# Kernel optimization log

Hardware: AMD Instinct MI355X
Metric: run time of the kernel (lower is better)

The kernel has to match this reference:

```python
import jax, jax.numpy as jnp
import numpy as np

B, N, D, E = 4, 8192, 8, 128
SCALE = float(1.0 / np.sqrt(E))  # torch MHA scaling, n_heads=1 -> head_dim=E


def _attn_dir(X, idx, mask, Wq, Wk, Wv, ipw, ipb, ow, ob):
    # X: [B,N,E]; idx, mask: [B,N,D]. Sequence per node = [self] + padded neighbors.
    neigh = jax.vmap(lambda x, i: x[i])(X, idx)               # [B,N,D,E] gather
    seq = jnp.concatenate([X[:, :, None, :], neigh], axis=2)  # [B,N,1+D,E]
    m = jnp.concatenate([jnp.ones(mask.shape[:2] + (1,), bool), mask.astype(bool)], axis=2)
    wq, wk, wv = jnp.split(ipw, 3, axis=0)                    # torch in_proj_weight [3E,E]
    bq, bk, bv = jnp.split(ipb, 3)
    # custom pre-projections (X @ W), then torch MHA in_proj (x @ w.T + b)
    q = (X @ Wq) @ wq.T + bq                                  # [B,N,E]; only self row queried
    k = (seq @ Wk) @ wk.T + bk                                # [B,N,1+D,E]
    v = (seq @ Wv) @ wv.T + bv                                # [B,N,1+D,E]
    scores = jnp.einsum('bne,bnse->bns', q, k) * SCALE
    scores = jnp.where(m, scores, jnp.finfo(scores.dtype).min)
    w = jax.nn.softmax(scores, axis=-1)
    ctx = jnp.einsum('bns,bnse->bne', w, v)
    return ctx @ ow.T + ob                                    # MHA out_proj


def setup_inputs():
    key = jax.random.key(0)
    ks = jax.random.split(key, 26)
    f32 = jnp.float32
    inp = {
        "X": jax.random.normal(ks[0], (B, N, E), f32),
        "in_idx": jax.random.randint(ks[1], (B, N, D), 0, N, dtype=jnp.int32),
        "out_idx": jax.random.randint(ks[2], (B, N, D), 0, N, dtype=jnp.int32),
        "in_mask": jax.random.randint(ks[3], (B, N, D), 0, 2, dtype=jnp.int32),
        "out_mask": jax.random.randint(ks[4], (B, N, D), 0, 2, dtype=jnp.int32),
    }
    i = 5
    for pfx in ("in_", "out_"):
        inp[pfx + "Wq"] = jax.random.uniform(ks[i], (E, E), f32) * 0.1; i += 1
        inp[pfx + "Wk"] = jax.random.uniform(ks[i], (E, E), f32) * 0.1; i += 1
        inp[pfx + "Wv"] = jax.random.uniform(ks[i], (E, E), f32) * 0.1; i += 1
        inp[pfx + "ipw"] = jax.random.normal(ks[i], (3 * E, E), f32) * 0.05; i += 1
        inp[pfx + "ipb"] = jax.random.normal(ks[i], (3 * E,), f32) * 0.02; i += 1
        inp[pfx + "ow"] = jax.random.normal(ks[i], (E, E), f32) * 0.05; i += 1
        inp[pfx + "ob"] = jax.random.normal(ks[i], (E,), f32) * 0.02; i += 1
    inp["lin_w"] = jax.random.normal(ks[i], (E, 2 * E), f32) * 0.05; i += 1
    inp["lin_b"] = jax.random.normal(ks[i], (E,), f32) * 0.02
    return inp


def reference(X, in_idx, out_idx, in_mask, out_mask,
              in_Wq, in_Wk, in_Wv, in_ipw, in_ipb, in_ow, in_ob,
              out_Wq, out_Wk, out_Wv, out_ipw, out_ipb, out_ow, out_ob,
              lin_w, lin_b):
    a_in = _attn_dir(X, in_idx, in_mask, in_Wq, in_Wk, in_Wv, in_ipw, in_ipb, in_ow, in_ob)
    a_out = _attn_dir(X, out_idx, out_mask, out_Wq, out_Wk, out_Wv, out_ipw, out_ipb, out_ow, out_ob)
    h = jnp.concatenate([a_in, a_out], axis=-1) @ lin_w.T + lin_b  # [B,N,E]
    return jax.nn.elu(h)
```

## Files before the change

### kernel.cpp

```cpp
#include <hip/hip_runtime.h>
#include <math.h>

#define NNODE 32768
constexpr float SCALE = 0.08838834764831845f;

typedef unsigned short u16;
typedef __bf16 bf16x8 __attribute__((ext_vector_type(8)));
typedef __bf16 bf16x2 __attribute__((ext_vector_type(2)));
typedef float f32x4 __attribute__((ext_vector_type(4)));

__device__ __forceinline__ u16 f2bf(float f) {
    unsigned u = __float_as_uint(f);
    u += 0x7fff + ((u >> 16) & 1);
    return (u16)(u >> 16);
}
__device__ __forceinline__ unsigned pack2bf(float lo, float hi) {
    return (unsigned)f2bf(lo) | ((unsigned)f2bf(hi) << 16);
}
__device__ __forceinline__ void unpack8(uint4 u, float* f) {
    f[0] = __uint_as_float(u.x << 16);  f[1] = __uint_as_float(u.x & 0xffff0000u);
    f[2] = __uint_as_float(u.y << 16);  f[3] = __uint_as_float(u.y & 0xffff0000u);
    f[4] = __uint_as_float(u.z << 16);  f[5] = __uint_as_float(u.z & 0xffff0000u);
    f[6] = __uint_as_float(u.w << 16);  f[7] = __uint_as_float(u.w & 0xffff0000u);
}
__device__ __forceinline__ float dot2bf(unsigned a, unsigned b, float c) {
#if __has_builtin(__builtin_amdgcn_fdot2_f32_bf16)
    union { unsigned u; bf16x2 v; } ua, ub;
    ua.u = a; ub.u = b;
    return __builtin_amdgcn_fdot2_f32_bf16(ua.v, ub.v, c, false);
#else
    float al = __uint_as_float(a << 16), ah = __uint_as_float(a & 0xffff0000u);
    float bl = __uint_as_float(b << 16), bh = __uint_as_float(b & 0xffff0000u);
    return fmaf(ah, bh, fmaf(al, bl, c));
#endif
}
__device__ __forceinline__ float dot8bf(uint4 a, uint4 b, float c) {
    c = dot2bf(a.x, b.x, c);
    c = dot2bf(a.y, b.y, c);
    c = dot2bf(a.z, b.z, c);
    c = dot2bf(a.w, b.w, c);
    return c;
}
__device__ __forceinline__ float dot128(const float* __restrict__ a,
                                        const float* __restrict__ b) {
    float s = 0.f;
    #pragma unroll
    for (int c = 0; c < 128; c += 4) {
        float4 x = *(const float4*)&a[c];
        float4 y = *(const float4*)&b[c];
        s = fmaf(x.x, y.x, s); s = fmaf(x.y, y.y, s);
        s = fmaf(x.z, y.z, s); s = fmaf(x.w, y.w, s);
    }
    return s;
}

__device__ __forceinline__ void gl_lds16(const void* g, void* l) {
    __builtin_amdgcn_global_load_lds(
        (const __attribute__((address_space(1))) unsigned int*)(uintptr_t)g,
        (__attribute__((address_space(3))) unsigned int*)(unsigned int)(uintptr_t)l,
        16, 0, 0);
}

__global__ __launch_bounds__(256) void wprep1(
    const float* __restrict__ ipw_in, const float* __restrict__ ipw_out,
    const float* __restrict__ Wq_in, const float* __restrict__ Wk_in,
    const float* __restrict__ Wv_in,
    const float* __restrict__ Wq_out, const float* __restrict__ Wk_out,
    const float* __restrict__ Wv_out,
    const float* __restrict__ ow_in, const float* __restrict__ ow_out,
    const float* __restrict__ lin_w,
    float* __restrict__ Af, float* __restrict__ Bmf,
    float* __restrict__ Wtf, float* __restrict__ RTf)
{
    int t = blockIdx.x * 256 + threadIdx.x;
    int i = t >> 7, j = t & 127;
    int task = blockIdx.y, dir = task & 1, kind = task >> 1;
    if (kind < 3) {
        const float* ipw = dir ? ipw_out : ipw_in;
        const float* W; const float* w; float* outp;
        if (kind == 0)      { W = dir ? Wq_out : Wq_in; w = ipw;          outp = Af;  }
        else if (kind == 1) { W = dir ? Wk_out : Wk_in; w = ipw + 16384;  outp = Bmf; }
        else                { W = dir ? Wv_out : Wv_in; w = ipw + 32768;  outp = Wtf; }
        outp[dir * 16384 + i * 128 + j] = dot128(W + i * 128, w + j * 128);
    } else {
        const float* ow = dir ? ow_out : ow_in;
        const float* lw = lin_w + i * 256 + dir * 128;
        float s = 0.f;
        #pragma unroll
        for (int e = 0; e < 128; e += 4) {
            float4 l4 = *(const float4*)&lw[e];
            s = fmaf(ow[e * 128 + j],       l4.x, s);
            s = fmaf(ow[(e + 1) * 128 + j], l4.y, s);
            s = fmaf(ow[(e + 2) * 128 + j], l4.z, s);
            s = fmaf(ow[(e + 3) * 128 + j], l4.w, s);
        }
        RTf[dir * 16384 + i * 128 + j] = s;
    }
}

__global__ __launch_bounds__(256) void wprep2(
    const float* __restrict__ Af, const float* __restrict__ Bmf,
    const float* __restrict__ Wtf, const float* __restrict__ RTf,
    const float* __restrict__ ipb_in, const float* __restrict__ ipb_out,
    const float* __restrict__ lin_w, const float* __restrict__ lin_b,
    const float* __restrict__ ob_in, const float* __restrict__ ob_out,
    u16* __restrict__ Bcat, u16* __restrict__ QfT,
    float* __restrict__ ycat, float* __restrict__ bfin)
{
    int task = blockIdx.y;
    int t = blockIdx.x * 256 + threadIdx.x;
    if (task < 2) {
        int dir = task, i = t >> 7, j = t & 127;
        float s = dot128(Af + dir * 16384 + j * 128, Bmf + dir * 16384 + i * 128);
        Bcat[(size_t)(dir * 128 + i) * 128 + j] = f2bf(s * SCALE);
    } else if (task < 4) {
        int dir = task - 2, i = t >> 7, j = t & 127;
        float s = dot128(Wtf + dir * 16384 + j * 128, RTf + dir * 16384 + i * 128);
        QfT[(size_t)i * 256 + dir * 128 + j] = f2bf(s);
    } else {
        if (t < 256) {
            int dir = t >> 7, d = t & 127;
            const float* bq = dir ? ipb_out : ipb_in;
            const float* rb = Bmf + dir * 16384 + d * 128;
            float s = 0.f;
            for (int f = 0; f < 128; ++f) s = fmaf(rb[f], bq[f], s);
            ycat[t] = s * SCALE;
        } else if (t < 384) {
            int g = t - 256;
            float s = lin_b[g];
            #pragma unroll
            for (int dir = 0; dir < 2; ++dir) {
                const float* bv = (dir ? ipb_out : ipb_in) + 256;
                const float* rt = RTf + dir * 16384 + g * 128;
                const float* ob = dir ? ob_out : ob_in;
                const float* lw = lin_w + g * 256 + dir * 128;
                for (int c = 0; c < 128; ++c)
                    s += bv[c] * rt[c] + ob[c] * lw[c];
            }
            bfin[g] = s;
        }
    }
}

template<int NT>
__global__ __launch_bounds__(256) void gemm_y(
    const float* __restrict__ X,
    const u16* __restrict__ BT,
    const float* __restrict__ bias,
    u16* __restrict__ C, u16* __restrict__ Xb)
{
    __shared__ __align__(16) u16 As[128 * 128];
    __shared__ __align__(16) u16 Bs[128 * 128];
    const int tid  = threadIdx.x;
    const int lane = tid & 63;
    const int wid  = tid >> 6;
    const int bm  = blockIdx.x * 128;
    const int wr = wid >> 1, wc = wid & 1;
    const int l15 = lane & 15, l4 = lane >> 4;

    #pragma unroll
    for (int i = 0; i < 8; ++i) {
        int c = i * 256 + tid;
        int r = c >> 4, cb = c & 15;
        const float* src = &X[(size_t)(bm + r) * 128 + cb * 8];
        float4 f0 = *(const float4*)src;
        float4 f1 = *(const float4*)(src + 4);
        uint4 pk;
        pk.x = pack2bf(f0.x, f0.y); pk.y = pack2bf(f0.z, f0.w);
        pk.z = pack2bf(f1.x, f1.y); pk.w = pack2bf(f1.z, f1.w);
        *(uint4*)&As[r * 128 + ((cb ^ (r & 7)) * 8)] = pk;
        *(uint4*)&Xb[(size_t)(bm + r) * 128 + cb * 8] = pk;
    }
    __syncthreads();
    bf16x8 a[4][4];
    #pragma unroll
    for (int ks = 0; ks < 4; ++ks)
        #pragma unroll
        for (int mr = 0; mr < 4; ++mr) {
            int r = wr * 64 + mr * 16 + l15;
            int kb = ks * 4 + l4;
            a[ks][mr] = *(const bf16x8*)((const char*)As + r * 256 + ((kb ^ (r & 7)) << 4));
        }

    #pragma unroll
    for (int nt = 0; nt < NT; ++nt) {
        int bn = nt * 128;
        __syncthreads();
        #pragma unroll
        for (int i = 0; i < 8; ++i) {
            int c = i * 256 + tid;
            int r = c >> 4, cb = c & 15;
            gl_lds16(&BT[(size_t)(bn + r) * 128 + 8 * (cb ^ (r & 7))],
                     &Bs[(size_t)(c - lane) * 8]);
        }
        __syncthreads();

        f32x4 acc[4][4] = {};
        #pragma unroll
        for (int ks = 0; ks < 4; ++ks) {
            bf16x8 bfr[4];
            #pragma unroll
            for (int nc = 0; nc < 4; ++nc) {
                int r = wc * 64 + nc * 16 + l15;
                int kb = ks * 4 + l4;
                bfr[nc] = *(const bf16x8*)((const char*)Bs + r * 256 + ((kb ^ (r & 7)) << 4));
            }
            #pragma unroll
            for (int mr = 0; mr < 4; ++mr)
                #pragma unroll
                for (int nc = 0; nc < 4; ++nc)
                    acc[mr][nc] = __builtin_amdgcn_mfma_f32_16x16x32_bf16(
                        a[ks][mr], bfr[nc], acc[mr][nc], 0, 0, 0);
        }
        #pragma unroll
        for (int nc = 0; nc < 4; ++nc) {
            int col = bn + wc * 64 + nc * 16 + l15;
            float bv = bias[col];
            #pragma unroll
            for (int mr = 0; mr < 4; ++mr)
                #pragma unroll
                for (int j = 0; j < 4; ++j) {
                    int row = bm + wr * 64 + mr * 16 + l4 * 4 + j;
                    C[(size_t)row * 256 + col] = f2bf(acc[mr][nc][j] + bv);
                }
        }
    }
}

__global__ __launch_bounds__(256) void attn_out(
    const u16* __restrict__ Y, const u16* __restrict__ Xb,
    const int* __restrict__ in_idx, const int* __restrict__ out_idx,
    const int* __restrict__ in_mask, const int* __restrict__ out_mask,
    const u16* __restrict__ QfT, const float* __restrict__ bfin,
    float* __restrict__ Cout)
{
    __shared__ __align__(16) u16 XC[32 * 256];

    const int tid  = threadIdx.x;
    const int lane = tid & 63;
    const int wid  = tid >> 6;
    const int l15  = lane & 15, l4 = lane >> 4;

    const int bid  = blockIdx.x;
    const int b    = (bid & 7) >> 1;
    const int s    = ((bid >> 3) << 1) + (bid & 1);
    const int node0 = (b << 13) + s * 32;

    {
        const int g = tid >> 4, l = tid & 15;
        #pragma unroll
        for (int round = 0; round < 4; ++round) {
            const int item = round * 16 + g;
            const int r   = item & 31;
            const int dir = item >> 5;
            const int node = node0 + r;
            const int* idx = dir ? out_idx : in_idx;
            const int* msk = dir ? out_mask : in_mask;

            const int4 i0 = *(const int4*)&idx[(size_t)node * 8];
            const int4 i1 = *(const int4*)&idx[(size_t)node * 8 + 4];
            const int4 m0 = *(const int4*)&msk[(size_t)node * 8];
            const int4 m1 = *(const int4*)&msk[(size_t)node * 8 + 4];
            const int ii[8] = { i0.x, i0.y, i0.z, i0.w, i1.x, i1.y, i1.z, i1.w };
            const int mm[8] = { m0.x, m0.y, m0.z, m0.w, m1.x, m1.y, m1.z, m1.w };

            uint4 yv = *(const uint4*)&Y[(size_t)node * 256 + dir * 128 + l * 8];
            uint4 xv[9];
            xv[0] = *(const uint4*)&Xb[(size_t)node * 128 + l * 8];
            #pragma unroll
            for (int t2 = 0; t2 < 8; ++t2)
                xv[t2 + 1] = *(const uint4*)&Xb[(size_t)((b << 13) + ii[t2]) * 128 + l * 8];

            float sc[9];
            #pragma unroll
            for (int t2 = 0; t2 < 9; ++t2)
                sc[t2] = dot8bf(yv, xv[t2], 0.f);

            #pragma unroll
            for (int t2 = 0; t2 < 9; ++t2) {
                float x = sc[t2];
                x += __shfl_xor(x, 1);
                x += __shfl_xor(x, 2);
                x += __shfl_xor(x, 4);
                x += __shfl_xor(x, 8);
                sc[t2] = x;
            }
            #pragma unroll
            for (int t2 = 1; t2 < 9; ++t2)
                sc[t2] = mm[t2 - 1] ? sc[t2] : -1e30f;

            float m = sc[0];
            #pragma unroll
            for (int t2 = 1; t2 < 9; ++t2) m = fmaxf(m, sc[t2]);
            float w[9], wsum = 0.f;
            #pragma unroll
            for (int t2 = 0; t2 < 9; ++t2) { w[t2] = __expf(sc[t2] - m); wsum += w[t2]; }
            const float inv = 1.f / wsum;

            float acc[8] = {};
            #pragma unroll
            for (int t2 = 0; t2 < 9; ++t2) {
                float vf[8];
                unpack8(xv[t2], vf);
                #pragma unroll
                for (int j = 0; j < 8; ++j) acc[j] = fmaf(w[t2], vf[j], acc[j]);
            }
            uint4 o;
            o.x = pack2bf(acc[0] * inv, acc[1] * inv);
            o.y = pack2bf(acc[2] * inv, acc[3] * inv);
            o.z = pack2bf(acc[4] * inv, acc[5] * inv);
            o.w = pack2bf(acc[6] * inv, acc[7] * inv);
            const int chunk = (dir << 4) + l;
            *(uint4*)((char*)XC + r * 512 + ((chunk ^ (r & 7)) << 4)) = o;
        }
    }
    __syncthreads();

    {
        f32x4 acc[2][2] = {};
        #pragma unroll
        for (int ks = 0; ks < 8; ++ks) {
            bf16x8 a[2], bb[2];
            #pragma unroll
            for (int mr = 0; mr < 2; ++mr) {
                int r = mr * 16 + l15;
                int kb = ks * 4 + l4;
                a[mr] = *(const bf16x8*)((const char*)XC + r * 512 + ((kb ^ (r & 7)) << 4));
            }
            #pragma unroll
            for (int nc = 0; nc < 2; ++nc) {
                int col = wid * 32 + nc * 16 + l15;
                bb[nc] = *(const bf16x8*)&QfT[(size_t)col * 256 + (ks * 4 + l4) * 8];
            }
            #pragma unroll
            for (int mr = 0; mr < 2; ++mr)
                #pragma unroll
                for (int nc = 0; nc < 2; ++nc)
                    acc[mr][nc] = __builtin_amdgcn_mfma_f32_16x16x32_bf16(
                        a[mr], bb[nc], acc[mr][nc], 0, 0, 0);
        }
        #pragma unroll
        for (int nc = 0; nc < 2; ++nc) {
            int col = wid * 32 + nc * 16 + l15;
            float bv = bfin[col];
            #pragma unroll
            for (int mr = 0; mr < 2; ++mr)
                #pragma unroll
                for (int j = 0; j < 4; ++j) {
                    int row = mr * 16 + l4 * 4 + j;
                    float v = acc[mr][nc][j] + bv;
                    v = v > 0.f ? v : (__expf(v) - 1.f);
                    Cout[(size_t)(node0 + row) * 128 + col] = v;
                }
        }
    }
}

extern "C" void kernel_launch(void* const* d_in, const int* in_sizes, int n_in,
                              void* d_out, int out_size, void* d_ws, size_t ws_size,
                              hipStream_t stream) {
    const float* X        = (const float*)d_in[0];
    const int*   in_idx   = (const int*)d_in[1];
    const int*   out_idx  = (const int*)d_in[2];
    const int*   in_mask  = (const int*)d_in[3];
    const int*   out_mask = (const int*)d_in[4];
    const float* Wq_in  = (const float*)d_in[5];
    const float* Wk_in  = (const float*)d_in[6];
    const float* Wv_in  = (const float*)d_in[7];
    const float* ipw_in = (const float*)d_in[8];
    const float* ipb_in = (const float*)d_in[9];
    const float* ow_in  = (const float*)d_in[10];
    const float* ob_in  = (const float*)d_in[11];
    const float* Wq_out  = (const float*)d_in[12];
    const float* Wk_out  = (const float*)d_in[13];
    const float* Wv_out  = (const float*)d_in[14];
    const float* ipw_out = (const float*)d_in[15];
    const float* ipb_out = (const float*)d_in[16];
    const float* ow_out  = (const float*)d_in[17];
    const float* ob_out  = (const float*)d_in[18];
    const float* lin_w   = (const float*)d_in[19];
    const float* lin_b   = (const float*)d_in[20];

    char* wsb = (char*)d_ws;
    u16*   Xbw  = (u16*)(wsb + 0);
    u16*   Yw   = (u16*)(wsb + 8388608);
    u16*   Bcat = (u16*)(wsb + 25165824);
    u16*   QfT  = (u16*)(wsb + 25231360);
    float* Af   = (float*)(wsb + 25296896);
    float* Bmf  = (float*)(wsb + 25427968);
    float* Wtf  = (float*)(wsb + 25559040);
    float* RTf  = (float*)(wsb + 25690112);
    float* ycat = (float*)(wsb + 25821184);
    float* bfin = (float*)(wsb + 25822208);

    wprep1<<<dim3(64, 8), 256, 0, stream>>>(
        ipw_in, ipw_out, Wq_in, Wk_in, Wv_in, Wq_out, Wk_out, Wv_out,
        ow_in, ow_out, lin_w, Af, Bmf, Wtf, RTf);

    wprep2<<<dim3(64, 5), 256, 0, stream>>>(
        Af, Bmf, Wtf, RTf, ipb_in, ipb_out, lin_w, lin_b, ob_in, ob_out,
        Bcat, QfT, ycat, bfin);

    gemm_y<2><<<dim3(256, 1), 256, 0, stream>>>(X, Bcat, ycat, Yw, Xbw);

    attn_out<<<1024, 256, 0, stream>>>(
        Yw, Xbw, in_idx, out_idx, in_mask, out_mask,
        QfT, bfin, (float*)d_out);
}
```

Measured before the change: 65.22 us.

## Shrink gemm tile to 64 rows with direct B loads; use bf16 dot2 in attention

The Y-projection GEMM now uses 64-row blocks (512 blocks instead of 256), with each wave computing a 64x64 output tile. B fragments are read straight from global memory instead of being staged in shared memory across two N-tiles, which removes the B LDS buffer and its barriers and raises the block count. Separately, the attention weighted sum packs pairs of softmax weights to bf16 and uses dot2 instructions on permuted value pairs, cutting the FMA count. The dot2 path rounds the weights to bf16, which adds some precision loss. Direct global B loads depend on cache hits for reuse across blocks.

```diff
diff --git a/kernel.cpp b/kernel.cpp
--- a/kernel.cpp
+++ b/kernel.cpp
@@ -142,24 +142,21 @@
     }
 }
 
-template<int NT>
-__global__ __launch_bounds__(256) void gemm_y(
+__global__ __launch_bounds__(256) void gemm_y64(
     const float* __restrict__ X,
     const u16* __restrict__ BT,
     const float* __restrict__ bias,
     u16* __restrict__ C, u16* __restrict__ Xb)
 {
-    __shared__ __align__(16) u16 As[128 * 128];
-    __shared__ __align__(16) u16 Bs[128 * 128];
+    __shared__ __align__(16) u16 As[64 * 128];
     const int tid  = threadIdx.x;
     const int lane = tid & 63;
     const int wid  = tid >> 6;
-    const int bm  = blockIdx.x * 128;
-    const int wr = wid >> 1, wc = wid & 1;
     const int l15 = lane & 15, l4 = lane >> 4;
+    const int bm  = blockIdx.x * 64;
 
     #pragma unroll
-    for (int i = 0; i < 8; ++i) {
+    for (int i = 0; i < 4; ++i) {
         int c = i * 256 + tid;
         int r = c >> 4, cb = c & 15;
         const float* src = &X[(size_t)(bm + r) * 128 + cb * 8];
@@ -172,58 +169,40 @@
         *(uint4*)&Xb[(size_t)(bm + r) * 128 + cb * 8] = pk;
     }
     __syncthreads();
-    bf16x8 a[4][4];
+
+    f32x4 acc[4][4] = {};
     #pragma unroll
-    for (int ks = 0; ks < 4; ++ks)
+    for (int ks = 0; ks < 4; ++ks) {
+        bf16x8 a[4], bb[4];
+        #pragma unroll
+        for (int nc = 0; nc < 4; ++nc) {
+            int col = wid * 64 + nc * 16 + l15;
+            bb[nc] = *(const bf16x8*)&BT[(size_t)col * 128 + (ks * 4 + l4) * 8];
+        }
         #pragma unroll
         for (int mr = 0; mr < 4; ++mr) {
-            int r = wr * 64 + mr * 16 + l15;
+            int r = mr * 16 + l15;
             int kb = ks * 4 + l4;
-            a[ks][mr] = *(const bf16x8*)((const char*)As + r * 256 + ((kb ^ (r & 7)) << 4));
-        }
-
+            a[mr] = *(const bf16x8*)((const char*)As + r * 256 + ((kb ^ (r & 7)) << 4));
+        }
+        #pragma unroll
+        for (int mr = 0; mr < 4; ++mr)
+            #pragma unroll
+            for (int nc = 0; nc < 4; ++nc)
+                acc[mr][nc] = __builtin_amdgcn_mfma_f32_16x16x32_bf16(
+                    a[mr], bb[nc], acc[mr][nc], 0, 0, 0);
+    }
     #pragma unroll
-    for (int nt = 0; nt < NT; ++nt) {
-        int bn = nt * 128;
-        __syncthreads();
-        #pragma unroll
-        for (int i = 0; i < 8; ++i) {
-            int c = i * 256 + tid;
-            int r = c >> 4, cb = c & 15;
-            gl_lds16(&BT[(size_t)(bn + r) * 128 + 8 * (cb ^ (r & 7))],
-                     &Bs[(size_t)(c - lane) * 8]);
-        }
-        __syncthreads();
-
-        f32x4 acc[4][4] = {};
-        #pragma unroll
-        for (int ks = 0; ks < 4; ++ks) {
-            bf16x8 bfr[4];
-            #pragma unroll
-            for (int nc = 0; nc < 4; ++nc) {
-                int r = wc * 64 + nc * 16 + l15;
-                int kb = ks * 4 + l4;
-                bfr[nc] = *(const bf16x8*)((const char*)Bs + r * 256 + ((kb ^ (r & 7)) << 4));
-            }
-            #pragma unroll
-            for (int mr = 0; mr < 4; ++mr)
-                #pragma unroll
-                for (int nc = 0; nc < 4; ++nc)
-                    acc[mr][nc] = __builtin_amdgcn_mfma_f32_16x16x32_bf16(
-                        a[ks][mr], bfr[nc], acc[mr][nc], 0, 0, 0);
-        }
-        #pragma unroll
-        for (int nc = 0; nc < 4; ++nc) {
-            int col = bn + wc * 64 + nc * 16 + l15;
-            float bv = bias[col];
-            #pragma unroll
-            for (int mr = 0; mr < 4; ++mr)
-                #pragma unroll
-                for (int j = 0; j < 4; ++j) {
-                    int row = bm + wr * 64 + mr * 16 + l4 * 4 + j;
-                    C[(size_t)row * 256 + col] = f2bf(acc[mr][nc][j] + bv);
-                }
-        }
+    for (int nc = 0; nc < 4; ++nc) {
+        int col = wid * 64 + nc * 16 + l15;
+        float bv = bias[col];
+        #pragma unroll
+        for (int mr = 0; mr < 4; ++mr)
+            #pragma unroll
+            for (int j = 0; j < 4; ++j) {
+                int row = bm + mr * 16 + l4 * 4 + j;
+                C[(size_t)row * 256 + col] = f2bf(acc[mr][nc][j] + bv);
+            }
     }
 }
 
@@ -298,12 +277,26 @@
             const float inv = 1.f / wsum;
 
             float acc[8] = {};
-            #pragma unroll
-            for (int t2 = 0; t2 < 9; ++t2) {
+            unsigned wp[4] = { pack2bf(w[0], w[1]), pack2bf(w[2], w[3]),
+                               pack2bf(w[4], w[5]), pack2bf(w[6], w[7]) };
+            #pragma unroll
+            for (int p = 0; p < 4; ++p) {
+                uint4 A = xv[2 * p], B = xv[2 * p + 1];
+                unsigned q;
+                q = __builtin_amdgcn_perm(B.x, A.x, 0x05040100u); acc[0] = dot2bf(wp[p], q, acc[0]);
+                q = __builtin_amdgcn_perm(B.x, A.x, 0x07060302u); acc[1] = dot2bf(wp[p], q, acc[1]);
+                q = __builtin_amdgcn_perm(B.y, A.y, 0x05040100u); acc[2] = dot2bf(wp[p], q, acc[2]);
+                q = __builtin_amdgcn_perm(B.y, A.y, 0x07060302u); acc[3] = dot2bf(wp[p], q, acc[3]);
+                q = __builtin_amdgcn_perm(B.z, A.z, 0x05040100u); acc[4] = dot2bf(wp[p], q, acc[4]);
+                q = __builtin_amdgcn_perm(B.z, A.z, 0x07060302u); acc[5] = dot2bf(wp[p], q, acc[5]);
+                q = __builtin_amdgcn_perm(B.w, A.w, 0x05040100u); acc[6] = dot2bf(wp[p], q, acc[6]);
+                q = __builtin_amdgcn_perm(B.w, A.w, 0x07060302u); acc[7] = dot2bf(wp[p], q, acc[7]);
+            }
+            {
                 float vf[8];
-                unpack8(xv[t2], vf);
+                unpack8(xv[8], vf);
                 #pragma unroll
-                for (int j = 0; j < 8; ++j) acc[j] = fmaf(w[t2], vf[j], acc[j]);
+                for (int j = 0; j < 8; ++j) acc[j] = fmaf(w[8], vf[j], acc[j]);
             }
             uint4 o;
             o.x = pack2bf(acc[0] * inv, acc[1] * inv);
@@ -401,7 +394,7 @@
         Af, Bmf, Wtf, RTf, ipb_in, ipb_out, lin_w, lin_b, ob_in, ob_out,
         Bcat, QfT, ycat, bfin);
 
-    gemm_y<2><<<dim3(256, 1), 256, 0, stream>>>(X, Bcat, ycat, Yw, Xbw);
+    gemm_y64<<<512, 256, 0, stream>>>(X, Bcat, ycat, Yw, Xbw);
 
     attn_out<<<1024, 256, 0, stream>>>(
         Yw, Xbw, in_idx, out_idx, in_mask, out_mask,
```

After: 66.84 us. +2.5%, slower.

## Stage neighbor indices in LDS and double-buffer gather loads in attn_out

Applied to the files above, without the earlier changes.

Before the gather, the block cooperatively loads all neighbor indices and masks into shared memory. The four gather rounds are then split into explicit issue and compute phases with two register buffers, so the next round's Xb loads are in flight while the current round's softmax runs. The aim is to hide gather latency and cut the redundant per-thread index loads. The cost is higher register pressure from holding two sets of nine uint4 values, plus an extra barrier.

```diff
diff --git a/kernel.cpp b/kernel.cpp
--- a/kernel.cpp
+++ b/kernel.cpp
@@ -235,6 +235,7 @@
     float* __restrict__ Cout)
 {
     __shared__ __align__(16) u16 XC[32 * 256];
+    __shared__ __align__(16) int4 IDXb[256];
 
     const int tid  = threadIdx.x;
     const int lane = tid & 63;
@@ -247,73 +248,97 @@
     const int node0 = (b << 13) + s * 32;
 
     {
-        const int g = tid >> 4, l = tid & 15;
-        #pragma unroll
-        for (int round = 0; round < 4; ++round) {
-            const int item = round * 16 + g;
-            const int r   = item & 31;
-            const int dir = item >> 5;
-            const int node = node0 + r;
-            const int* idx = dir ? out_idx : in_idx;
-            const int* msk = dir ? out_mask : in_mask;
-
-            const int4 i0 = *(const int4*)&idx[(size_t)node * 8];
-            const int4 i1 = *(const int4*)&idx[(size_t)node * 8 + 4];
-            const int4 m0 = *(const int4*)&msk[(size_t)node * 8];
-            const int4 m1 = *(const int4*)&msk[(size_t)node * 8 + 4];
-            const int ii[8] = { i0.x, i0.y, i0.z, i0.w, i1.x, i1.y, i1.z, i1.w };
-            const int mm[8] = { m0.x, m0.y, m0.z, m0.w, m1.x, m1.y, m1.z, m1.w };
-
-            uint4 yv = *(const uint4*)&Y[(size_t)node * 256 + dir * 128 + l * 8];
-            uint4 xv[9];
-            xv[0] = *(const uint4*)&Xb[(size_t)node * 128 + l * 8];
-            #pragma unroll
-            for (int t2 = 0; t2 < 8; ++t2)
-                xv[t2 + 1] = *(const uint4*)&Xb[(size_t)((b << 13) + ii[t2]) * 128 + l * 8];
-
-            float sc[9];
-            #pragma unroll
-            for (int t2 = 0; t2 < 9; ++t2)
-                sc[t2] = dot8bf(yv, xv[t2], 0.f);
-
-            #pragma unroll
-            for (int t2 = 0; t2 < 9; ++t2) {
-                float x = sc[t2];
-                x += __shfl_xor(x, 1);
-                x += __shfl_xor(x, 2);
-                x += __shfl_xor(x, 4);
-                x += __shfl_xor(x, 8);
-                sc[t2] = x;
-            }
-            #pragma unroll
-            for (int t2 = 1; t2 < 9; ++t2)
-                sc[t2] = mm[t2 - 1] ? sc[t2] : -1e30f;
-
-            float m = sc[0];
-            #pragma unroll
-            for (int t2 = 1; t2 < 9; ++t2) m = fmaxf(m, sc[t2]);
-            float w[9], wsum = 0.f;
-            #pragma unroll
-            for (int t2 = 0; t2 < 9; ++t2) { w[t2] = __expf(sc[t2] - m); wsum += w[t2]; }
-            const float inv = 1.f / wsum;
-
-            float acc[8] = {};
-            #pragma unroll
-            for (int t2 = 0; t2 < 9; ++t2) {
-                float vf[8];
-                unpack8(xv[t2], vf);
-                #pragma unroll
-                for (int j = 0; j < 8; ++j) acc[j] = fmaf(w[t2], vf[j], acc[j]);
-            }
-            uint4 o;
-            o.x = pack2bf(acc[0] * inv, acc[1] * inv);
-            o.y = pack2bf(acc[2] * inv, acc[3] * inv);
-            o.z = pack2bf(acc[4] * inv, acc[5] * inv);
-            o.w = pack2bf(acc[6] * inv, acc[7] * inv);
-            const int chunk = (dir << 4) + l;
-            *(uint4*)((char*)XC + r * 512 + ((chunk ^ (r & 7)) << 4)) = o;
-        }
-    }
+        int e = tid;
+        int dir = e >> 7, rem = e & 127;
+        int node = rem >> 2, j = rem & 3;
+        const int* base = (j < 2) ? (dir ? out_idx : in_idx)
+                                  : (dir ? out_mask : in_mask);
+        IDXb[e] = *(const int4*)&base[(size_t)(node0 + node) * 8 + (j & 1) * 4];
+    }
+    __syncthreads();
+
+    const int g = tid >> 4, l = tid & 15;
+
+    uint4 yv[2];
+    uint4 xv[2][9];
+
+#define ISSUE(RR, BUF) do {                                                   \
+    const int item_ = (RR) * 16 + g;                                          \
+    const int nd_ = item_ & 31, dr_ = item_ >> 5;                             \
+    int4 i0_ = IDXb[dr_ * 128 + nd_ * 4 + 0];                                 \
+    int4 i1_ = IDXb[dr_ * 128 + nd_ * 4 + 1];                                 \
+    const int node_ = node0 + nd_;                                            \
+    yv[BUF] = *(const uint4*)&Y[(size_t)node_ * 256 + dr_ * 128 + l * 8];     \
+    xv[BUF][0] = *(const uint4*)&Xb[(size_t)node_ * 128 + l * 8];             \
+    xv[BUF][1] = *(const uint4*)&Xb[(size_t)((b << 13) + i0_.x) * 128 + l * 8]; \
+    xv[BUF][2] = *(const uint4*)&Xb[(size_t)((b << 13) + i0_.y) * 128 + l * 8]; \
+    xv[BUF][3] = *(const uint4*)&Xb[(size_t)((b << 13) + i0_.z) * 128 + l * 8]; \
+    xv[BUF][4] = *(const uint4*)&Xb[(size_t)((b << 13) + i0_.w) * 128 + l * 8]; \
+    xv[BUF][5] = *(const uint4*)&Xb[(size_t)((b << 13) + i1_.x) * 128 + l * 8]; \
+    xv[BUF][6] = *(const uint4*)&Xb[(size_t)((b << 13) + i1_.y) * 128 + l * 8]; \
+    xv[BUF][7] = *(const uint4*)&Xb[(size_t)((b << 13) + i1_.z) * 128 + l * 8]; \
+    xv[BUF][8] = *(const uint4*)&Xb[(size_t)((b << 13) + i1_.w) * 128 + l * 8]; \
+} while (0)
+
+#define COMPUTE(RR, BUF) do {                                                 \
+    const int item_ = (RR) * 16 + g;                                          \
+    const int nd_ = item_ & 31, dr_ = item_ >> 5;                             \
+    int4 mq0_ = IDXb[dr_ * 128 + nd_ * 4 + 2];                                \
+    int4 mq1_ = IDXb[dr_ * 128 + nd_ * 4 + 3];                                \
+    const int mm_[8] = { mq0_.x, mq0_.y, mq0_.z, mq0_.w,                      \
+                         mq1_.x, mq1_.y, mq1_.z, mq1_.w };                    \
+    float sc_[9];                                                             \
+    _Pragma("unroll")                                                         \
+    for (int t2 = 0; t2 < 9; ++t2)                                            \
+        sc_[t2] = dot8bf(yv[BUF], xv[BUF][t2], 0.f);                          \
+    _Pragma("unroll")                                                         \
+    for (int t2 = 0; t2 < 9; ++t2) {                                          \
+        float x_ = sc_[t2];                                                   \
+        x_ += __shfl_xor(x_, 1);                                              \
+        x_ += __shfl_xor(x_, 2);                                              \
+        x_ += __shfl_xor(x_, 4);                                              \
+        x_ += __shfl_xor(x_, 8);                                              \
+        sc_[t2] = x_;                                                         \
+    }                                                                         \
+    _Pragma("unroll")                                                         \
+    for (int t2 = 1; t2 < 9; ++t2)                                            \
+        sc_[t2] = mm_[t2 - 1] ? sc_[t2] : -1e30f;                             \
+    float m_ = sc_[0];                                                        \
+    _Pragma("unroll")                                                         \
+    for (int t2 = 1; t2 < 9; ++t2) m_ = fmaxf(m_, sc_[t2]);                   \
+    float w_[9], wsum_ = 0.f;                                                 \
+    _Pragma("unroll")                                                         \
+    for (int t2 = 0; t2 < 9; ++t2) { w_[t2] = __expf(sc_[t2] - m_); wsum_ += w_[t2]; } \
+    const float inv_ = 1.f / wsum_;                                           \
+    float acc_[8] = {};                                                       \
+    _Pragma("unroll")                                                         \
+    for (int t2 = 0; t2 < 9; ++t2) {                                          \
+        float vf_[8];                                                         \
+        unpack8(xv[BUF][t2], vf_);                                            \
+        _Pragma("unroll")                                                     \
+        for (int j_ = 0; j_ < 8; ++j_) acc_[j_] = fmaf(w_[t2], vf_[j_], acc_[j_]); \
+    }                                                                         \
+    uint4 o_;                                                                 \
+    o_.x = pack2bf(acc_[0] * inv_, acc_[1] * inv_);                           \
+    o_.y = pack2bf(acc_[2] * inv_, acc_[3] * inv_);                           \
+    o_.z = pack2bf(acc_[4] * inv_, acc_[5] * inv_);                           \
+    o_.w = pack2bf(acc_[6] * inv_, acc_[7] * inv_);                           \
+    const int chunk_ = (dr_ << 4) + l;                                        \
+    *(uint4*)((char*)XC + nd_ * 512 + ((chunk_ ^ (nd_ & 7)) << 4)) = o_;      \
+} while (0)
+
+    ISSUE(0, 0);
+    ISSUE(1, 1);
+    COMPUTE(0, 0);
+    ISSUE(2, 0);
+    COMPUTE(1, 1);
+    ISSUE(3, 1);
+    COMPUTE(2, 0);
+    COMPUTE(3, 1);
+
+#undef ISSUE
+#undef COMPUTE
+
     __syncthreads();
 
     {
```

Measured after the change: 66.43 us. About the same (+1.9%).

## Compute weight-prep matrix products with bf16 MFMA tiles and restructure bias folding

Applied to the files above, without the earlier changes.

The two weight-preparation kernels now compute each 128x128 weight product in a single block using bf16 MFMA with swizzled LDS tiles, replacing the scalar fp32 per-element dot products spread over many blocks. The bias-vector computation is refactored to derive ycat and bfin from the original weights instead of the intermediate fused matrices. This cuts scalar FMA work and launches far fewer blocks, but runs only 8 and 5 blocks, which leaves most CUs idle. Intermediate weight products are also rounded to bf16 before the second product, which adds error.

```diff
diff --git a/kernel.cpp b/kernel.cpp
--- a/kernel.cpp
+++ b/kernel.cpp
@@ -41,18 +41,6 @@
     c = dot2bf(a.w, b.w, c);
     return c;
 }
-__device__ __forceinline__ float dot128(const float* __restrict__ a,
-                                        const float* __restrict__ b) {
-    float s = 0.f;
-    #pragma unroll
-    for (int c = 0; c < 128; c += 4) {
-        float4 x = *(const float4*)&a[c];
-        float4 y = *(const float4*)&b[c];
-        s = fmaf(x.x, y.x, s); s = fmaf(x.y, y.y, s);
-        s = fmaf(x.z, y.z, s); s = fmaf(x.w, y.w, s);
-    }
-    return s;
-}
 
 __device__ __forceinline__ void gl_lds16(const void* g, void* l) {
     __builtin_amdgcn_global_load_lds(
@@ -61,7 +49,7 @@
         16, 0, 0);
 }
 
-__global__ __launch_bounds__(256) void wprep1(
+__global__ __launch_bounds__(256) void wprepA(
     const float* __restrict__ ipw_in, const float* __restrict__ ipw_out,
     const float* __restrict__ Wq_in, const float* __restrict__ Wk_in,
     const float* __restrict__ Wv_in,
@@ -72,72 +60,211 @@
     float* __restrict__ Af, float* __restrict__ Bmf,
     float* __restrict__ Wtf, float* __restrict__ RTf)
 {
-    int t = blockIdx.x * 256 + threadIdx.x;
-    int i = t >> 7, j = t & 127;
-    int task = blockIdx.y, dir = task & 1, kind = task >> 1;
+    __shared__ __align__(16) u16 As[128 * 128];
+    __shared__ __align__(16) u16 Bs[128 * 128];
+    const int tid = threadIdx.x, lane = tid & 63, wid = tid >> 6;
+    const int l15 = lane & 15, l4 = lane >> 4;
+    const int task = blockIdx.x, dir = task & 1, kind = task >> 1;
+
+    const float* ipw = dir ? ipw_out : ipw_in;
+    const float* Ag; int lda; const float* Bg; float* outp;
+    if (kind == 0)      { Ag = dir ? Wq_out : Wq_in; lda = 128; Bg = ipw;          outp = Af;  }
+    else if (kind == 1) { Ag = dir ? Wk_out : Wk_in; lda = 128; Bg = ipw + 16384;  outp = Bmf; }
+    else if (kind == 2) { Ag = dir ? Wv_out : Wv_in; lda = 128; Bg = ipw + 32768;  outp = Wtf; }
+    else                { Ag = lin_w + dir * 128;    lda = 256; Bg = dir ? ow_out : ow_in; outp = RTf; }
+    outp += dir * 16384;
+
+    #pragma unroll
+    for (int i = 0; i < 8; ++i) {
+        int c = i * 256 + tid, r = c >> 4, cb = c & 15;
+        const float* src = &Ag[(size_t)r * lda + cb * 8];
+        float4 f0 = *(const float4*)src, f1 = *(const float4*)(src + 4);
+        uint4 pk;
+        pk.x = pack2bf(f0.x, f0.y); pk.y = pack2bf(f0.z, f0.w);
+        pk.z = pack2bf(f1.x, f1.y); pk.w = pack2bf(f1.z, f1.w);
+        *(uint4*)&As[r * 128 + ((cb ^ (r & 7)) * 8)] = pk;
+    }
     if (kind < 3) {
-        const float* ipw = dir ? ipw_out : ipw_in;
-        const float* W; const float* w; float* outp;
-        if (kind == 0)      { W = dir ? Wq_out : Wq_in; w = ipw;          outp = Af;  }
-        else if (kind == 1) { W = dir ? Wk_out : Wk_in; w = ipw + 16384;  outp = Bmf; }
-        else                { W = dir ? Wv_out : Wv_in; w = ipw + 32768;  outp = Wtf; }
-        outp[dir * 16384 + i * 128 + j] = dot128(W + i * 128, w + j * 128);
+        #pragma unroll
+        for (int i = 0; i < 8; ++i) {
+            int c = i * 256 + tid, r = c >> 4, cb = c & 15;
+            const float* src = &Bg[(size_t)r * 128 + cb * 8];
+            float4 f0 = *(const float4*)src, f1 = *(const float4*)(src + 4);
+            uint4 pk;
+            pk.x = pack2bf(f0.x, f0.y); pk.y = pack2bf(f0.z, f0.w);
+            pk.z = pack2bf(f1.x, f1.y); pk.w = pack2bf(f1.z, f1.w);
+            *(uint4*)&Bs[r * 128 + ((cb ^ (r & 7)) * 8)] = pk;
+        }
     } else {
-        const float* ow = dir ? ow_out : ow_in;
-        const float* lw = lin_w + i * 256 + dir * 128;
-        float s = 0.f;
-        #pragma unroll
-        for (int e = 0; e < 128; e += 4) {
-            float4 l4 = *(const float4*)&lw[e];
-            s = fmaf(ow[e * 128 + j],       l4.x, s);
-            s = fmaf(ow[(e + 1) * 128 + j], l4.y, s);
-            s = fmaf(ow[(e + 2) * 128 + j], l4.z, s);
-            s = fmaf(ow[(e + 3) * 128 + j], l4.w, s);
-        }
-        RTf[dir * 16384 + i * 128 + j] = s;
-    }
-}
-
-__global__ __launch_bounds__(256) void wprep2(
+        #pragma unroll
+        for (int i = 0; i < 8; ++i) {
+            int c = i * 256 + tid, f = c >> 4, cb = c & 15;
+            u16 tmp[8];
+            #pragma unroll
+            for (int q = 0; q < 8; ++q)
+                tmp[q] = f2bf(Bg[(size_t)(cb * 8 + q) * 128 + f]);
+            *(uint4*)&Bs[f * 128 + ((cb ^ (f & 7)) * 8)] = *(const uint4*)tmp;
+        }
+    }
+    __syncthreads();
+
+    const int wr = wid >> 1, wc = wid & 1;
+    f32x4 acc[4][4] = {};
+    #pragma unroll
+    for (int ks = 0; ks < 4; ++ks) {
+        bf16x8 a[4], b[4];
+        #pragma unroll
+        for (int mr = 0; mr < 4; ++mr) {
+            int r = wr * 64 + mr * 16 + l15, kb = ks * 4 + l4;
+            a[mr] = *(const bf16x8*)((const char*)As + r * 256 + ((kb ^ (r & 7)) << 4));
+        }
+        #pragma unroll
+        for (int nc = 0; nc < 4; ++nc) {
+            int r = wc * 64 + nc * 16 + l15, kb = ks * 4 + l4;
+            b[nc] = *(const bf16x8*)((const char*)Bs + r * 256 + ((kb ^ (r & 7)) << 4));
+        }
+        #pragma unroll
+        for (int mr = 0; mr < 4; ++mr)
+            #pragma unroll
+            for (int nc = 0; nc < 4; ++nc)
+                acc[mr][nc] = __builtin_amdgcn_mfma_f32_16x16x32_bf16(
+                    a[mr], b[nc], acc[mr][nc], 0, 0, 0);
+    }
+    #pragma unroll
+    for (int nc = 0; nc < 4; ++nc) {
+        int col = wc * 64 + nc * 16 + l15;
+        #pragma unroll
+        for (int mr = 0; mr < 4; ++mr)
+            #pragma unroll
+            for (int j = 0; j < 4; ++j)
+                outp[(size_t)(wr * 64 + mr * 16 + l4 * 4 + j) * 128 + col] = acc[mr][nc][j];
+    }
+}
+
+__global__ __launch_bounds__(256) void wprepB(
     const float* __restrict__ Af, const float* __restrict__ Bmf,
     const float* __restrict__ Wtf, const float* __restrict__ RTf,
+    const float* __restrict__ ipw_in, const float* __restrict__ ipw_out,
     const float* __restrict__ ipb_in, const float* __restrict__ ipb_out,
+    const float* __restrict__ ow_in, const float* __restrict__ ow_out,
+    const float* __restrict__ ob_in, const float* __restrict__ ob_out,
+    const float* __restrict__ Wk_in, const float* __restrict__ Wk_out,
     const float* __restrict__ lin_w, const float* __restrict__ lin_b,
-    const float* __restrict__ ob_in, const float* __restrict__ ob_out,
     u16* __restrict__ Bcat, u16* __restrict__ QfT,
     float* __restrict__ ycat, float* __restrict__ bfin)
 {
-    int task = blockIdx.y;
-    int t = blockIdx.x * 256 + threadIdx.x;
-    if (task < 2) {
-        int dir = task, i = t >> 7, j = t & 127;
-        float s = dot128(Af + dir * 16384 + j * 128, Bmf + dir * 16384 + i * 128);
-        Bcat[(size_t)(dir * 128 + i) * 128 + j] = f2bf(s * SCALE);
-    } else if (task < 4) {
-        int dir = task - 2, i = t >> 7, j = t & 127;
-        float s = dot128(Wtf + dir * 16384 + j * 128, RTf + dir * 16384 + i * 128);
-        QfT[(size_t)i * 256 + dir * 128 + j] = f2bf(s);
+    __shared__ __align__(16) u16 As[128 * 128];
+    __shared__ __align__(16) u16 Bs[128 * 128];
+    const int tid = threadIdx.x, lane = tid & 63, wid = tid >> 6;
+    const int l15 = lane & 15, l4 = lane >> 4;
+    const int task = blockIdx.x;
+
+    if (task < 4) {
+        const int dir = task & 1;
+        const bool isB = (task < 2);
+        const float* Ag = (isB ? Bmf : RTf) + dir * 16384;
+        const float* Bg = (isB ? Af  : Wtf) + dir * 16384;
+        #pragma unroll
+        for (int i = 0; i < 8; ++i) {
+            int c = i * 256 + tid, r = c >> 4, cb = c & 15;
+            const float* srcA = &Ag[(size_t)r * 128 + cb * 8];
+            float4 a0 = *(const float4*)srcA, a1 = *(const float4*)(srcA + 4);
+            uint4 pa;
+            pa.x = pack2bf(a0.x, a0.y); pa.y = pack2bf(a0.z, a0.w);
+            pa.z = pack2bf(a1.x, a1.y); pa.w = pack2bf(a1.z, a1.w);
+            *(uint4*)&As[r * 128 + ((cb ^ (r & 7)) * 8)] = pa;
+            const float* srcB = &Bg[(size_t)r * 128 + cb * 8];
+            float4 b0 = *(const float4*)srcB, b1 = *(const float4*)(srcB + 4);
+            uint4 pb;
+            pb.x = pack2bf(b0.x, b0.y); pb.y = pack2bf(b0.z, b0.w);
+            pb.z = pack2bf(b1.x, b1.y); pb.w = pack2bf(b1.z, b1.w);
+            *(uint4*)&Bs[r * 128 + ((cb ^ (r & 7)) * 8)] = pb;
+        }
+        __syncthreads();
+
+        const int wr = wid >> 1, wc = wid & 1;
+        f32x4 acc[4][4] = {};
+        #pragma unroll
+        for (int ks = 0; ks < 4; ++ks) {
+            bf16x8 a[4], b[4];
+            #pragma unroll
+            for (int mr = 0; mr < 4; ++mr) {
+                int r = wr * 64 + mr * 16 + l15, kb = ks * 4 + l4;
+                a[mr] = *(const bf16x8*)((const char*)As + r * 256 + ((kb ^ (r & 7)) << 4));
+            }
+            #pragma unroll
+            for (int nc = 0; nc < 4; ++nc) {
+                int r = wc * 64 + nc * 16 + l15, kb = ks * 4 + l4;
+                b[nc] = *(const bf16x8*)((const char*)Bs + r * 256 + ((kb ^ (r & 7)) << 4));
+            }
+            #pragma unroll
+            for (int mr = 0; mr < 4; ++mr)
+                #pragma unroll
+                for (int nc = 0; nc < 4; ++nc)
+                    acc[mr][nc] = __builtin_amdgcn_mfma_f32_16x16x32_bf16(
+                        a[mr], b[nc], acc[mr][nc], 0, 0, 0);
+        }
+        #pragma unroll
+        for (int nc = 0; nc < 4; ++nc) {
+            int col = wc * 64 + nc * 16 + l15;
+            #pragma unroll
+            for (int mr = 0; mr < 4; ++mr)
+                #pragma unroll
+                for (int j = 0; j < 4; ++j) {
+                    int row = wr * 64 + mr * 16 + l4 * 4 + j;
+                    float v = acc[mr][nc][j];
+                    if (isB)
+                        Bcat[(size_t)(dir * 128 + row) * 128 + col] = f2bf(v * SCALE);
+                    else
+                        QfT[(size_t)row * 256 + dir * 128 + col] = f2bf(v);
+                }
+        }
     } else {
-        if (t < 256) {
-            int dir = t >> 7, d = t & 127;
+        float* sv = (float*)As;
+        {
+            int dir = tid >> 7, e = tid & 127;
+            const float* wk = (dir ? ipw_out : ipw_in) + 16384;
             const float* bq = dir ? ipb_out : ipb_in;
-            const float* rb = Bmf + dir * 16384 + d * 128;
             float s = 0.f;
-            for (int f = 0; f < 128; ++f) s = fmaf(rb[f], bq[f], s);
-            ycat[t] = s * SCALE;
-        } else if (t < 384) {
-            int g = t - 256;
-            float s = lin_b[g];
-            #pragma unroll
-            for (int dir = 0; dir < 2; ++dir) {
-                const float* bv = (dir ? ipb_out : ipb_in) + 256;
-                const float* rt = RTf + dir * 16384 + g * 128;
-                const float* ob = dir ? ob_out : ob_in;
-                const float* lw = lin_w + g * 256 + dir * 128;
-                for (int c = 0; c < 128; ++c)
-                    s += bv[c] * rt[c] + ob[c] * lw[c];
-            }
-            bfin[g] = s;
+            for (int f = 0; f < 128; ++f) s = fmaf(wk[(size_t)f * 128 + e], bq[f], s);
+            sv[tid] = s;
+            const float* ow = dir ? ow_out : ow_in;
+            const float* bv = (dir ? ipb_out : ipb_in) + 256;
+            float u = 0.f;
+            #pragma unroll
+            for (int f = 0; f < 128; f += 4) {
+                float4 o4 = *(const float4*)&ow[(size_t)e * 128 + f];
+                float4 b4 = *(const float4*)&bv[f];
+                u = fmaf(o4.x, b4.x, u); u = fmaf(o4.y, b4.y, u);
+                u = fmaf(o4.z, b4.z, u); u = fmaf(o4.w, b4.w, u);
+            }
+            sv[256 + tid] = u + (dir ? ob_out : ob_in)[e];
+        }
+        __syncthreads();
+        {
+            int dir = tid >> 7, d = tid & 127;
+            const float* Wk = dir ? Wk_out : Wk_in;
+            const float* v = sv + dir * 128;
+            float s = 0.f;
+            #pragma unroll
+            for (int e = 0; e < 128; e += 4) {
+                float4 w4 = *(const float4*)&Wk[(size_t)d * 128 + e];
+                s = fmaf(w4.x, v[e], s);     s = fmaf(w4.y, v[e + 1], s);
+                s = fmaf(w4.z, v[e + 2], s); s = fmaf(w4.w, v[e + 3], s);
+            }
+            ycat[tid] = s * SCALE;
+        }
+        if (tid < 128) {
+            const float* lw = lin_w + (size_t)tid * 256;
+            const float* z = sv + 256;
+            float s = lin_b[tid];
+            #pragma unroll
+            for (int e2 = 0; e2 < 256; e2 += 4) {
+                float4 l4v = *(const float4*)&lw[e2];
+                s = fmaf(l4v.x, z[e2], s);     s = fmaf(l4v.y, z[e2 + 1], s);
+                s = fmaf(l4v.z, z[e2 + 2], s); s = fmaf(l4v.w, z[e2 + 3], s);
+            }
+            bfin[tid] = s;
         }
     }
 }
@@ -393,12 +520,13 @@
     float* ycat = (float*)(wsb + 25821184);
     float* bfin = (float*)(wsb + 25822208);
 
-    wprep1<<<dim3(64, 8), 256, 0, stream>>>(
+    wprepA<<<8, 256, 0, stream>>>(
         ipw_in, ipw_out, Wq_in, Wk_in, Wv_in, Wq_out, Wk_out, Wv_out,
         ow_in, ow_out, lin_w, Af, Bmf, Wtf, RTf);
 
-    wprep2<<<dim3(64, 5), 256, 0, stream>>>(
-        Af, Bmf, Wtf, RTf, ipb_in, ipb_out, lin_w, lin_b, ob_in, ob_out,
+    wprepB<<<5, 256, 0, stream>>>(
+        Af, Bmf, Wtf, RTf, ipw_in, ipw_out, ipb_in, ipb_out,
+        ow_in, ow_out, ob_in, ob_out, Wk_in, Wk_out, lin_w, lin_b,
         Bcat, QfT, ycat, bfin);
 
     gemm_y<2><<<dim3(256, 1), 256, 0, stream>>>(X, Bcat, ycat, Yw, Xbw);
```

New measurement: 66.53 us. +2.0%, slower.
